# Kernel optimization log

Hardware: AMD Instinct MI355X
Metric: run time of the kernel (lower is better)

The kernel has to match this reference:

```python
import jax, jax.numpy as jnp
import numpy as np
from math import sqrt

B, D, H, HD, PF, K = 256, 1024, 8, 128, 2, 4
P = PF * D        # 2048, up-projected dim
HID = H * HD      # 1024
EPS = 1e-5


def _lin_w(key, out_d, in_d):
    return jax.random.normal(key, (out_d, in_d), jnp.float32) / np.sqrt(in_d)


def setup_inputs() -> dict:
    key = jax.random.key(0)
    ks = jax.random.split(key, 16)
    inp = {
        "seq": jax.random.normal(ks[0], (B, D), jnp.float32),
        "c_tm1": jax.random.normal(ks[1], (B, H, HD, HD), jnp.float32) * 0.1,
        "n_tm1": jnp.ones((B, H, HD), jnp.float32),
        "m_tm1": jnp.zeros((B, H), jnp.float32),
        # norms
        "ln_w": jnp.ones((D,), jnp.float32), "ln_b": jnp.zeros((D,), jnp.float32),
        "gn_w": jnp.ones((HID,), jnp.float32), "gn_b": jnp.zeros((HID,), jnp.float32),
        # linears (torch Linear: y = x @ W.T + b)
        "up_l_w": _lin_w(ks[2], P, D), "up_l_b": jnp.zeros((P,), jnp.float32),
        "up_r_w": _lin_w(ks[3], HID, D), "up_r_b": jnp.zeros((HID,), jnp.float32),
        "down_w": _lin_w(ks[4], D, HID), "down_b": jnp.zeros((D,), jnp.float32),
        "Wi_w": _lin_w(ks[5], H, P), "Wi_b": jnp.zeros((H,), jnp.float32),
        "Wf_w": _lin_w(ks[6], H, P), "Wf_b": jnp.zeros((H,), jnp.float32),
        "Wo_w": _lin_w(ks[7], HID, P), "Wo_b": jnp.zeros((HID,), jnp.float32),
        "Wq_w": _lin_w(ks[8], HID, P), "Wq_b": jnp.zeros((HID,), jnp.float32),
        "Wk_w": _lin_w(ks[9], HID, P), "Wk_b": jnp.zeros((HID,), jnp.float32),
        "Wv_w": _lin_w(ks[10], HID, P), "Wv_b": jnp.zeros((HID,), jnp.float32),
        # causal conv1d (1->1 channel, kernel K) and 1x1 skip conv (no bias)
        "conv_w": jax.random.normal(ks[11], (K,), jnp.float32) / np.sqrt(K),
        "conv_b": jnp.zeros((), jnp.float32),
        "skip_w": _lin_w(ks[12], HID, P),
    }
    return inp


def _layernorm(x, w, b):
    mu = jnp.mean(x, -1, keepdims=True)
    var = jnp.mean(jnp.square(x - mu), -1, keepdims=True)
    return (x - mu) * jax.lax.rsqrt(var + EPS) * w + b


def reference(seq, c_tm1, n_tm1, m_tm1, ln_w, ln_b, gn_w, gn_b,
              up_l_w, up_l_b, up_r_w, up_r_b, down_w, down_b,
              Wi_w, Wi_b, Wf_w, Wf_b, Wo_w, Wo_b,
              Wq_w, Wq_b, Wk_w, Wk_b, Wv_w, Wv_b,
              conv_w, conv_b, skip_w):
    x_n = _layernorm(seq, ln_w, ln_b)                     # [B, D]
    x_t = x_n @ up_l_w.T + up_l_b                         # [B, P]
    r_t = x_n @ up_r_w.T + up_r_b                         # [B, HID]

    # causal conv along feature axis: left-pad K-1, cross-correlate
    xp = jnp.pad(x_t, ((0, 0), (K - 1, 0)))
    x_c = sum(conv_w[j] * xp[:, j:j + P] for j in range(K)) + conv_b
    x_c = jax.nn.silu(x_c)                                # [B, P]

    q = (x_c @ Wq_w.T + Wq_b).reshape(B, H, HD)
    k = (x_c @ Wk_w.T + Wk_b).reshape(B, H, HD) / sqrt(HD)
    v = (x_t @ Wv_w.T + Wv_b).reshape(B, H, HD)
    i_t = x_c @ Wi_w.T + Wi_b                             # [B, H]
    f_t = x_c @ Wf_w.T + Wf_b                             # [B, H]
    o_t = jax.nn.sigmoid(x_t @ Wo_w.T + Wo_b)             # [B, HID]

    # stabilized exponential gating
    m_t = jnp.maximum(f_t + m_tm1, i_t)
    i_g = jnp.exp(i_t - m_t)
    f_g = jnp.exp(f_t - m_t + m_tm1)

    vk = jnp.einsum('bhd,bhp->bhdp', v, k)                # outer-product write
    c_t = f_g[:, :, None, None] * c_tm1 + i_g[:, :, None, None] * vk
    n_t = f_g[:, :, None] * n_tm1 + i_g[:, :, None] * k

    num = jnp.einsum('bhdp,bhp->bhd', c_t, q)
    den = jnp.maximum(jnp.einsum('bhd,bhd->bh', n_t, q), 1.0)
    h_t = o_t * (num / den[:, :, None]).reshape(B, HID)   # [B, HID]

    # GroupNorm(H groups) over channels
    hg = h_t.reshape(B, H, HD)
    mu = jnp.mean(hg, -1, keepdims=True)
    var = jnp.mean(jnp.square(hg - mu), -1, keepdims=True)
    hn = ((hg - mu) * jax.lax.rsqrt(var + EPS)).reshape(B, HID) * gn_w + gn_b

    out = hn + x_c @ skip_w.T                             # 1x1 skip conv
    out = out * jax.nn.silu(r_t)
    out = out @ down_w.T + down_b
    return out + seq, c_t, n_t, m_t
```

## Files before the change

### kernel.cpp

```cpp
#include <hip/hip_runtime.h>
#include <hip/hip_bf16.h>
#include <math.h>

#define B 256
#define D 1024
#define H 8
#define HD 128
#define P 2048
#define HID 1024
#define EPS 1e-5f

typedef __hip_bfloat16 bf16;
typedef short short8 __attribute__((ext_vector_type(8)));
typedef float f32x4 __attribute__((ext_vector_type(4)));

#define AS1C(p) ((const __attribute__((address_space(1))) void*)(p))
#define AS3(p)  ((__attribute__((address_space(3))) void*)(p))

__global__ __launch_bounds__(256) void zero_kernel(float* __restrict__ p) {
    const int i = blockIdx.x * 256 + threadIdx.x;
    ((float4*)p)[i] = float4{0.f, 0.f, 0.f, 0.f};
}

struct CvtSegs { const float* src[8]; bf16* dst[8]; };

__global__ __launch_bounds__(256) void convert_kernel(CvtSegs cs) {
    const int idx = blockIdx.x * 256 + threadIdx.x;
    const float* src; bf16* dst; int base;
    if      (idx <  524288) { src = cs.src[0]; dst = cs.dst[0]; base = 0; }
    else if (idx <  786432) { src = cs.src[1]; dst = cs.dst[1]; base = 524288; }
    else if (idx < 1310720) { src = cs.src[2]; dst = cs.dst[2]; base = 786432; }
    else if (idx < 1835008) { src = cs.src[3]; dst = cs.dst[3]; base = 1310720; }
    else if (idx < 2359296) { src = cs.src[4]; dst = cs.dst[4]; base = 1835008; }
    else if (idx < 2883584) { src = cs.src[5]; dst = cs.dst[5]; base = 2359296; }
    else if (idx < 3407872) { src = cs.src[6]; dst = cs.dst[6]; base = 2883584; }
    else                    { src = cs.src[7]; dst = cs.dst[7]; base = 3407872; }
    const int j = idx - base;
    const float4 v = ((const float4*)src)[j];
    union { bf16 h[4]; uint2 u; } tmp;
    tmp.h[0] = __float2bfloat16(v.x); tmp.h[1] = __float2bfloat16(v.y);
    tmp.h[2] = __float2bfloat16(v.z); tmp.h[3] = __float2bfloat16(v.w);
    *(uint2*)&dst[4 * j] = tmp.u;
}

__global__ __launch_bounds__(256) void ln_kernel(
    const float* __restrict__ seq, const float* __restrict__ w,
    const float* __restrict__ b, bf16* __restrict__ xn)
{
    const int row = blockIdx.x;
    const int tid = threadIdx.x;
    const int lane = tid & 63, wv = tid >> 6;
    const float* x = seq + (size_t)row * D;
    __shared__ float red[8];

    float vals[4];
    float s = 0.f, s2 = 0.f;
#pragma unroll
    for (int i = 0; i < 4; ++i) {
        float v = x[tid + 256 * i];
        vals[i] = v; s += v; s2 += v * v;
    }
#pragma unroll
    for (int off = 32; off; off >>= 1) {
        s  += __shfl_down(s, off, 64);
        s2 += __shfl_down(s2, off, 64);
    }
    if (lane == 0) { red[wv] = s; red[4 + wv] = s2; }
    __syncthreads();
    const float tot  = red[0] + red[1] + red[2] + red[3];
    const float tot2 = red[4] + red[5] + red[6] + red[7];
    const float mu = tot * (1.f / D);
    const float var = tot2 * (1.f / D) - mu * mu;
    const float rs = rsqrtf(var + EPS);
#pragma unroll
    for (int i = 0; i < 4; ++i) {
        const int c = tid + 256 * i;
        xn[(size_t)row * D + c] = __float2bfloat16((vals[i] - mu) * rs * w[c] + b[c]);
    }
}

struct Segs {
    const bf16* A[5];
    const bf16* W[5];
    float* O[5];
    int ostride[5];
};

__global__ __launch_bounds__(256) void gemm_bf16_sk(Segs segs, int K, int KS) {
    const int nt = blockIdx.x;
    const int seg = nt >> 4, nloc = nt & 15;
    const int m0 = blockIdx.y * 64;
    const int k0 = blockIdx.z * KS;
    const bf16* Ab = segs.A[seg];
    const bf16* Wb = segs.W[seg] + (size_t)(nloc * 64) * K;

    __shared__ bf16 As[2][64 * 64];
    __shared__ bf16 Bs[2][64 * 64];

    const int tid = threadIdx.x;
    const int srow = tid >> 3;
    const int scol = ((tid & 7) ^ (srow & 7)) * 8;
    const bf16* gA = Ab + (size_t)(m0 + srow) * K + k0 + scol;
    const bf16* gB = Wb + (size_t)srow * K + k0 + scol;
    const size_t rowK32 = (size_t)32 * K;

    const int lane = tid & 63, wave = tid >> 6;
    const int wm = (wave >> 1) * 32, wn = (wave & 1) * 32;
    const int fr = lane & 15, kq = lane >> 4;
    const int s0 = ((kq ^ (fr & 7)) * 8);
    const int aoff = (wm + fr) * 64 + s0;
    const int boff = (wn + fr) * 64 + s0;

    f32x4 acc00 = {0.f, 0.f, 0.f, 0.f};
    f32x4 acc01 = {0.f, 0.f, 0.f, 0.f};
    f32x4 acc10 = {0.f, 0.f, 0.f, 0.f};
    f32x4 acc11 = {0.f, 0.f, 0.f, 0.f};

    const int nIter = KS >> 6;

    __builtin_amdgcn_global_load_lds(AS1C(gA),          AS3(&As[0][tid * 8]),        16, 0, 0);
    __builtin_amdgcn_global_load_lds(AS1C(gA + rowK32), AS3(&As[0][2048 + tid * 8]), 16, 0, 0);
    __builtin_amdgcn_global_load_lds(AS1C(gB),          AS3(&Bs[0][tid * 8]),        16, 0, 0);
    __builtin_amdgcn_global_load_lds(AS1C(gB + rowK32), AS3(&Bs[0][2048 + tid * 8]), 16, 0, 0);

    int buf = 0;
    for (int it = 0; it < nIter; ++it) {
        __syncthreads();
        if (it + 1 < nIter) {
            const int ko = (it + 1) * 64;
            __builtin_amdgcn_global_load_lds(AS1C(gA + ko),          AS3(&As[buf ^ 1][tid * 8]),        16, 0, 0);
            __builtin_amdgcn_global_load_lds(AS1C(gA + ko + rowK32), AS3(&As[buf ^ 1][2048 + tid * 8]), 16, 0, 0);
            __builtin_amdgcn_global_load_lds(AS1C(gB + ko),          AS3(&Bs[buf ^ 1][tid * 8]),        16, 0, 0);
            __builtin_amdgcn_global_load_lds(AS1C(gB + ko + rowK32), AS3(&Bs[buf ^ 1][2048 + tid * 8]), 16, 0, 0);
        }
        {
            const short8 a0 = *(const short8*)&As[buf][aoff];
            const short8 a1 = *(const short8*)&As[buf][aoff + 1024];
            const short8 b0 = *(const short8*)&Bs[buf][boff];
            const short8 b1 = *(const short8*)&Bs[buf][boff + 1024];
            acc00 = __builtin_amdgcn_mfma_f32_16x16x32_bf16(a0, b0, acc00, 0, 0, 0);
            acc01 = __builtin_amdgcn_mfma_f32_16x16x32_bf16(a0, b1, acc01, 0, 0, 0);
            acc10 = __builtin_amdgcn_mfma_f32_16x16x32_bf16(a1, b0, acc10, 0, 0, 0);
            acc11 = __builtin_amdgcn_mfma_f32_16x16x32_bf16(a1, b1, acc11, 0, 0, 0);
        }
        {
            const short8 a0 = *(const short8*)&As[buf][aoff ^ 32];
            const short8 a1 = *(const short8*)&As[buf][(aoff + 1024) ^ 32];
            const short8 b0 = *(const short8*)&Bs[buf][boff ^ 32];
            const short8 b1 = *(const short8*)&Bs[buf][(boff + 1024) ^ 32];
            acc00 = __builtin_amdgcn_mfma_f32_16x16x32_bf16(a0, b0, acc00, 0, 0, 0);
            acc01 = __builtin_amdgcn_mfma_f32_16x16x32_bf16(a0, b1, acc01, 0, 0, 0);
            acc10 = __builtin_amdgcn_mfma_f32_16x16x32_bf16(a1, b0, acc10, 0, 0, 0);
            acc11 = __builtin_amdgcn_mfma_f32_16x16x32_bf16(a1, b1, acc11, 0, 0, 0);
        }
        buf ^= 1;
    }

    float* Ob = segs.O[seg] + nloc * 64 + wn;
    const int ost = segs.ostride[seg];
    const int r0 = m0 + wm + (lane >> 4) * 4;
    const int c0 = lane & 15;
#pragma unroll
    for (int r = 0; r < 4; ++r) {
        atomicAdd(&Ob[(size_t)(r0 + r) * ost + c0],           acc00[r]);
        atomicAdd(&Ob[(size_t)(r0 + r) * ost + 16 + c0],      acc01[r]);
        atomicAdd(&Ob[(size_t)(r0 + r + 16) * ost + c0],      acc10[r]);
        atomicAdd(&Ob[(size_t)(r0 + r + 16) * ost + 16 + c0], acc11[r]);
    }
}

__global__ __launch_bounds__(256) void conv_kernel(
    const float* __restrict__ xtacc, const float* __restrict__ ulb,
    const float* __restrict__ cw, const float* __restrict__ cb,
    bf16* __restrict__ xt_bf, float* __restrict__ xc, bf16* __restrict__ xc_bf)
{
    const int idx = blockIdx.x * 256 + threadIdx.x;
    const int b = idx >> 11, i = idx & 2047;
    const float* row = xtacc + (size_t)b * P;
    const float x0 = row[i] + ulb[i];
    xt_bf[idx] = __float2bfloat16(x0);
    float acc = cb[0] + cw[3] * x0;
    if (i >= 1) acc = fmaf(cw[2], row[i - 1] + ulb[i - 1], acc);
    if (i >= 2) acc = fmaf(cw[1], row[i - 2] + ulb[i - 2], acc);
    if (i >= 3) acc = fmaf(cw[0], row[i - 3] + ulb[i - 3], acc);
    const float sv = acc / (1.f + expf(-acc));
    xc[idx] = sv;
    xc_bf[idx] = __float2bfloat16(sv);
}

__global__ __launch_bounds__(256) void if_kernel(
    const float* __restrict__ xc,
    const float* __restrict__ Wi, const float* __restrict__ Wib,
    const float* __restrict__ Wf, const float* __restrict__ Wfb,
    float* __restrict__ it, float* __restrict__ ft)
{
    const int blk = blockIdx.x;
    const int b = blk >> 3, h = blk & 7;
    const int tid = threadIdx.x;
    const int lane = tid & 63, wv = tid >> 6;
    const float* x = xc + (size_t)b * P;
    const float* wi = Wi + (size_t)h * P;
    const float* wf = Wf + (size_t)h * P;
    float pi = 0.f, pf = 0.f;
    for (int p = tid; p < P; p += 256) {
        const float xv = x[p];
        pi = fmaf(xv, wi[p], pi);
        pf = fmaf(xv, wf[p], pf);
    }
    __shared__ float red[8];
#pragma unroll
    for (int off = 32; off; off >>= 1) {
        pi += __shfl_down(pi, off, 64);
        pf += __shfl_down(pf, off, 64);
    }
    if (lane == 0) { red[wv] = pi; red[4 + wv] = pf; }
    __syncthreads();
    if (tid == 0) {
        it[blk] = red[0] + red[1] + red[2] + red[3] + Wib[h];
        ft[blk] = red[4] + red[5] + red[6] + red[7] + Wfb[h];
    }
}

__global__ __launch_bounds__(256) void gate_kernel(
    const float* __restrict__ c_tm1, const float* __restrict__ n_tm1,
    const float* __restrict__ m_tm1, const float* __restrict__ it_a,
    const float* __restrict__ ft_a,
    const float* __restrict__ qacc, const float* __restrict__ kacc,
    const float* __restrict__ vacc, const float* __restrict__ oacc,
    const float* __restrict__ sacc, const float* __restrict__ racc,
    const float* __restrict__ qb, const float* __restrict__ kb,
    const float* __restrict__ vb, const float* __restrict__ ob,
    const float* __restrict__ rb,
    const float* __restrict__ gn_w, const float* __restrict__ gn_b,
    float* __restrict__ c_out, float* __restrict__ n_out,
    float* __restrict__ m_out, bf16* __restrict__ y)
{
    const int blk = blockIdx.x;
    const int b = blk >> 3, h = blk & 7;
    const int tid = threadIdx.x;
    const int lane = tid & 63, wv = tid >> 6;
    const float kscale = 0.08838834764831845f;

    __shared__ float sk_[128], sq_[128], sv_[128], snum[128];
    __shared__ float red[8];

    const float it = it_a[blk], ft = ft_a[blk], mp = m_tm1[blk];
    const float mt = fmaxf(ft + mp, it);
    const float ig = expf(it - mt);
    const float fg = expf(ft - mt + mp);
    if (tid == 0) m_out[blk] = mt;

    const int col0 = h * HD;
    const int hid_off = b * HID + col0;
    float den_p = 0.f;
    if (tid < 128) {
        const int col = col0 + tid;
        const float kd = (kacc[hid_off + tid] + kb[col]) * kscale;
        const float qd = qacc[hid_off + tid] + qb[col];
        sk_[tid] = kd; sq_[tid] = qd;
        sv_[tid] = vacc[hid_off + tid] + vb[col];
        const float nn = fg * n_tm1[(size_t)blk * HD + tid] + ig * kd;
        n_out[(size_t)blk * HD + tid] = nn;
        den_p = nn * qd;
    }
    __syncthreads();
#pragma unroll
    for (int off = 32; off; off >>= 1) den_p += __shfl_down(den_p, off, 64);
    if (lane == 0) red[wv] = den_p;
    __syncthreads();
    const float den = fmaxf(red[0] + red[1] + red[2] + red[3], 1.0f);

    const float k0 = sk_[2 * lane], k1 = sk_[2 * lane + 1];
    const float q0 = sq_[2 * lane], q1 = sq_[2 * lane + 1];
    const size_t cbase = (size_t)blk * (HD * HD);
#pragma unroll 4
    for (int r = 0; r < 32; ++r) {
        const int d = r * 4 + wv;
        const float2 c2 = *(const float2*)(c_tm1 + cbase + d * HD + 2 * lane);
        const float a = ig * sv_[d];
        const float c0v = fmaf(fg, c2.x, a * k0);
        const float c1v = fmaf(fg, c2.y, a * k1);
        float2 st; st.x = c0v; st.y = c1v;
        *(float2*)(c_out + cbase + d * HD + 2 * lane) = st;
        float psum = c0v * q0 + c1v * q1;
#pragma unroll
        for (int off = 32; off; off >>= 1) psum += __shfl_down(psum, off, 64);
        if (lane == 0) snum[d] = psum;
    }
    __syncthreads();

    float hval = 0.f, s1 = 0.f, s2 = 0.f;
    if (tid < 128) {
        const int col = col0 + tid;
        const float ot = 1.f / (1.f + expf(-(oacc[hid_off + tid] + ob[col])));
        hval = ot * snum[tid] / den;
        s1 = hval; s2 = hval * hval;
    }
#pragma unroll
    for (int off = 32; off; off >>= 1) {
        s1 += __shfl_down(s1, off, 64);
        s2 += __shfl_down(s2, off, 64);
    }
    if (lane == 0) { red[wv] = s1; red[4 + wv] = s2; }
    __syncthreads();
    const float mu = (red[0] + red[1] + red[2] + red[3]) * (1.f / HD);
    const float ms = (red[4] + red[5] + red[6] + red[7]) * (1.f / HD);
    const float var = ms - mu * mu;
    if (tid < 128) {
        const int col = col0 + tid;
        const float hn = (hval - mu) * rsqrtf(var + EPS) * gn_w[col] + gn_b[col];
        const float sr = racc[hid_off + tid] + rb[col];
        const float silu_r = sr / (1.f + expf(-sr));
        y[hid_off + tid] = __float2bfloat16((hn + sacc[hid_off + tid]) * silu_r);
    }
}

__global__ __launch_bounds__(256) void e3_kernel(
    const float* __restrict__ dacc, const float* __restrict__ db,
    const float* __restrict__ seq, float* __restrict__ out)
{
    const int i = blockIdx.x * 256 + threadIdx.x;
    const float4 d = ((const float4*)dacc)[i];
    const float4 s = ((const float4*)seq)[i];
    const float4 bb = ((const float4*)db)[i & 255];
    float4 o;
    o.x = d.x + s.x + bb.x; o.y = d.y + s.y + bb.y;
    o.z = d.z + s.z + bb.z; o.w = d.w + s.w + bb.w;
    ((float4*)out)[i] = o;
}

extern "C" void kernel_launch(void* const* d_in, const int* in_sizes, int n_in,
                              void* d_out, int out_size, void* d_ws, size_t ws_size,
                              hipStream_t stream) {
    const float* seq    = (const float*)d_in[0];
    const float* c_tm1  = (const float*)d_in[1];
    const float* n_tm1  = (const float*)d_in[2];
    const float* m_tm1  = (const float*)d_in[3];
    const float* ln_w   = (const float*)d_in[4];
    const float* ln_b   = (const float*)d_in[5];
    const float* gn_w   = (const float*)d_in[6];
    const float* gn_b   = (const float*)d_in[7];
    const float* up_l_w = (const float*)d_in[8];
    const float* up_l_b = (const float*)d_in[9];
    const float* up_r_w = (const float*)d_in[10];
    const float* up_r_b = (const float*)d_in[11];
    const float* down_w = (const float*)d_in[12];
    const float* down_b = (const float*)d_in[13];
    const float* Wi_w   = (const float*)d_in[14];
    const float* Wi_b   = (const float*)d_in[15];
    const float* Wf_w   = (const float*)d_in[16];
    const float* Wf_b   = (const float*)d_in[17];
    const float* Wo_w   = (const float*)d_in[18];
    const float* Wo_b   = (const float*)d_in[19];
    const float* Wq_w   = (const float*)d_in[20];
    const float* Wq_b   = (const float*)d_in[21];
    const float* Wk_w   = (const float*)d_in[22];
    const float* Wk_b   = (const float*)d_in[23];
    const float* Wv_w   = (const float*)d_in[24];
    const float* Wv_b   = (const float*)d_in[25];
    const float* conv_w = (const float*)d_in[26];
    const float* conv_b = (const float*)d_in[27];
    const float* skip_w = (const float*)d_in[28];

    float* ws = (float*)d_ws;
    float* xtacc = ws;
    float* racc  = ws + 524288;
    float* qacc  = ws + 786432;
    float* kacc  = ws + 1048576;
    float* vacc  = ws + 1310720;
    float* oacc  = ws + 1572864;
    float* sacc  = ws + 1835008;
    float* dacc  = ws + 2097152;
    float* itb   = ws + 2359296;
    float* ftb   = ws + 2361344;
    bf16* yb_bf   = (bf16*)(ws + 2363392);
    bf16* down_bf = (bf16*)(ws + 2494464);

    float* out0  = (float*)d_out;
    float* c_out = out0 + 262144;
    float* n_out = out0 + 33816576;
    float* m_out = out0 + 34078720;

    bf16* wbuf   = (bf16*)c_out;
    bf16* upl_bf = wbuf;
    bf16* upr_bf = wbuf + 2097152;
    bf16* wq_bf  = wbuf + 3145728;
    bf16* wk_bf  = wbuf + 5242880;
    bf16* wv_bf  = wbuf + 7340032;
    bf16* wo_bf  = wbuf + 9437184;
    bf16* wsk_bf = wbuf + 11534336;
    bf16* xn_bf  = wbuf + 13631488;
    bf16* xt_bf  = wbuf + 13893632;
    bf16* xc_bf  = wbuf + 14417920;
    float* xc_f  = (float*)(wbuf + 14942208);

    zero_kernel<<<2304, 256, 0, stream>>>(ws);

    CvtSegs cv;
    cv.src[0] = up_l_w; cv.dst[0] = upl_bf;
    cv.src[1] = up_r_w; cv.dst[1] = upr_bf;
    cv.src[2] = Wq_w;   cv.dst[2] = wq_bf;
    cv.src[3] = Wk_w;   cv.dst[3] = wk_bf;
    cv.src[4] = Wv_w;   cv.dst[4] = wv_bf;
    cv.src[5] = Wo_w;   cv.dst[5] = wo_bf;
    cv.src[6] = skip_w; cv.dst[6] = wsk_bf;
    cv.src[7] = down_w; cv.dst[7] = down_bf;
    convert_kernel<<<14336, 256, 0, stream>>>(cv);

    ln_kernel<<<B, 256, 0, stream>>>(seq, ln_w, ln_b, xn_bf);

    Segs g1{};
    g1.A[0] = xn_bf; g1.W[0] = upl_bf;               g1.O[0] = xtacc;        g1.ostride[0] = P;
    g1.A[1] = xn_bf; g1.W[1] = upl_bf + 1024 * 1024; g1.O[1] = xtacc + 1024; g1.ostride[1] = P;
    g1.A[2] = xn_bf; g1.W[2] = upr_bf;               g1.O[2] = racc;         g1.ostride[2] = HID;
    gemm_bf16_sk<<<dim3(48, 4, 4), 256, 0, stream>>>(g1, 1024, 256);

    conv_kernel<<<(B * P) / 256, 256, 0, stream>>>(
        xtacc, up_l_b, conv_w, conv_b, xt_bf, xc_f, xc_bf);

    Segs g2{};
    g2.A[0] = xc_bf; g2.W[0] = wq_bf;  g2.O[0] = qacc; g2.ostride[0] = HID;
    g2.A[1] = xc_bf; g2.W[1] = wk_bf;  g2.O[1] = kacc; g2.ostride[1] = HID;
    g2.A[2] = xt_bf; g2.W[2] = wv_bf;  g2.O[2] = vacc; g2.ostride[2] = HID;
    g2.A[3] = xt_bf; g2.W[3] = wo_bf;  g2.O[3] = oacc; g2.ostride[3] = HID;
    g2.A[4] = xc_bf; g2.W[4] = wsk_bf; g2.O[4] = sacc; g2.ostride[4] = HID;
    gemm_bf16_sk<<<dim3(80, 4, 2), 256, 0, stream>>>(g2, 2048, 1024);

    if_kernel<<<B * H, 256, 0, stream>>>(xc_f, Wi_w, Wi_b, Wf_w, Wf_b, itb, ftb);

    gate_kernel<<<B * H, 256, 0, stream>>>(
        c_tm1, n_tm1, m_tm1, itb, ftb,
        qacc, kacc, vacc, oacc, sacc, racc,
        Wq_b, Wk_b, Wv_b, Wo_b, up_r_b, gn_w, gn_b,
        c_out, n_out, m_out, yb_bf);

    Segs g3{};
    g3.A[0] = yb_bf; g3.W[0] = down_bf; g3.O[0] = dacc; g3.ostride[0] = HID;
    gemm_bf16_sk<<<dim3(16, 4, 4), 256, 0, stream>>>(g3, 1024, 256);

    e3_kernel<<<256, 256, 0, stream>>>(dacc, down_b, seq, out0);
}
```

Before: 393.4 us.

## Fuse fp32-to-bf16 weight conversion into GEMM loads and vectorize gate kernel

Drops the separate weight conversion kernel. The GEMM now loads fp32 weight tiles into registers, converts them to bf16 and writes them swizzled into LDS, overlapping this with the MFMA work through register prefetch. This avoids writing and re-reading about 14M bf16 weights each call. Split-K and M-tiling now re-read the fp32 weights (twice the bytes) several times. The gate kernel's c-state update also switches to float4 accesses with batched xor-shuffle row reductions.

```diff
diff --git a/kernel.cpp b/kernel.cpp
--- a/kernel.cpp
+++ b/kernel.cpp
@@ -20,27 +20,6 @@
 __global__ __launch_bounds__(256) void zero_kernel(float* __restrict__ p) {
     const int i = blockIdx.x * 256 + threadIdx.x;
     ((float4*)p)[i] = float4{0.f, 0.f, 0.f, 0.f};
-}
-
-struct CvtSegs { const float* src[8]; bf16* dst[8]; };
-
-__global__ __launch_bounds__(256) void convert_kernel(CvtSegs cs) {
-    const int idx = blockIdx.x * 256 + threadIdx.x;
-    const float* src; bf16* dst; int base;
-    if      (idx <  524288) { src = cs.src[0]; dst = cs.dst[0]; base = 0; }
-    else if (idx <  786432) { src = cs.src[1]; dst = cs.dst[1]; base = 524288; }
-    else if (idx < 1310720) { src = cs.src[2]; dst = cs.dst[2]; base = 786432; }
-    else if (idx < 1835008) { src = cs.src[3]; dst = cs.dst[3]; base = 1310720; }
-    else if (idx < 2359296) { src = cs.src[4]; dst = cs.dst[4]; base = 1835008; }
-    else if (idx < 2883584) { src = cs.src[5]; dst = cs.dst[5]; base = 2359296; }
-    else if (idx < 3407872) { src = cs.src[6]; dst = cs.dst[6]; base = 2883584; }
-    else                    { src = cs.src[7]; dst = cs.dst[7]; base = 3407872; }
-    const int j = idx - base;
-    const float4 v = ((const float4*)src)[j];
-    union { bf16 h[4]; uint2 u; } tmp;
-    tmp.h[0] = __float2bfloat16(v.x); tmp.h[1] = __float2bfloat16(v.y);
-    tmp.h[2] = __float2bfloat16(v.z); tmp.h[3] = __float2bfloat16(v.w);
-    *(uint2*)&dst[4 * j] = tmp.u;
 }
 
 __global__ __launch_bounds__(256) void ln_kernel(
@@ -81,10 +60,19 @@
 
 struct Segs {
     const bf16* A[5];
-    const bf16* W[5];
+    const float* W[5];
     float* O[5];
     int ostride[5];
 };
+
+static __device__ inline short8 cvt8(float4 a, float4 b) {
+    union { bf16 h[8]; short8 s; } u;
+    u.h[0] = __float2bfloat16(a.x); u.h[1] = __float2bfloat16(a.y);
+    u.h[2] = __float2bfloat16(a.z); u.h[3] = __float2bfloat16(a.w);
+    u.h[4] = __float2bfloat16(b.x); u.h[5] = __float2bfloat16(b.y);
+    u.h[6] = __float2bfloat16(b.z); u.h[7] = __float2bfloat16(b.w);
+    return u.s;
+}
 
 __global__ __launch_bounds__(256) void gemm_bf16_sk(Segs segs, int K, int KS) {
     const int nt = blockIdx.x;
@@ -92,17 +80,20 @@
     const int m0 = blockIdx.y * 64;
     const int k0 = blockIdx.z * KS;
     const bf16* Ab = segs.A[seg];
-    const bf16* Wb = segs.W[seg] + (size_t)(nloc * 64) * K;
+    const float* Wb = segs.W[seg] + (size_t)(nloc * 64) * K;
 
     __shared__ bf16 As[2][64 * 64];
     __shared__ bf16 Bs[2][64 * 64];
 
     const int tid = threadIdx.x;
     const int srow = tid >> 3;
-    const int scol = ((tid & 7) ^ (srow & 7)) * 8;
-    const bf16* gA = Ab + (size_t)(m0 + srow) * K + k0 + scol;
-    const bf16* gB = Wb + (size_t)srow * K + k0 + scol;
+    const int swz8 = ((tid & 7) ^ (srow & 7)) * 8;
+    const bf16* gA = Ab + (size_t)(m0 + srow) * K + k0 + swz8;
     const size_t rowK32 = (size_t)32 * K;
+    const float* gW0 = Wb + (size_t)srow * K + k0 + (tid & 7) * 8;
+    const float* gW1 = gW0 + rowK32;
+    const int wd0 = srow * 64 + swz8;
+    const int wd1 = (srow + 32) * 64 + swz8;
 
     const int lane = tid & 63, wave = tid >> 6;
     const int wm = (wave >> 1) * 32, wn = (wave & 1) * 32;
@@ -118,20 +109,26 @@
 
     const int nIter = KS >> 6;
 
+    float4 w00 = *(const float4*)(gW0);
+    float4 w01 = *(const float4*)(gW0 + 4);
+    float4 w10 = *(const float4*)(gW1);
+    float4 w11 = *(const float4*)(gW1 + 4);
     __builtin_amdgcn_global_load_lds(AS1C(gA),          AS3(&As[0][tid * 8]),        16, 0, 0);
     __builtin_amdgcn_global_load_lds(AS1C(gA + rowK32), AS3(&As[0][2048 + tid * 8]), 16, 0, 0);
-    __builtin_amdgcn_global_load_lds(AS1C(gB),          AS3(&Bs[0][tid * 8]),        16, 0, 0);
-    __builtin_amdgcn_global_load_lds(AS1C(gB + rowK32), AS3(&Bs[0][2048 + tid * 8]), 16, 0, 0);
+    *(short8*)&Bs[0][wd0] = cvt8(w00, w01);
+    *(short8*)&Bs[0][wd1] = cvt8(w10, w11);
 
     int buf = 0;
     for (int it = 0; it < nIter; ++it) {
         __syncthreads();
         if (it + 1 < nIter) {
             const int ko = (it + 1) * 64;
+            w00 = *(const float4*)(gW0 + ko);
+            w01 = *(const float4*)(gW0 + ko + 4);
+            w10 = *(const float4*)(gW1 + ko);
+            w11 = *(const float4*)(gW1 + ko + 4);
             __builtin_amdgcn_global_load_lds(AS1C(gA + ko),          AS3(&As[buf ^ 1][tid * 8]),        16, 0, 0);
             __builtin_amdgcn_global_load_lds(AS1C(gA + ko + rowK32), AS3(&As[buf ^ 1][2048 + tid * 8]), 16, 0, 0);
-            __builtin_amdgcn_global_load_lds(AS1C(gB + ko),          AS3(&Bs[buf ^ 1][tid * 8]),        16, 0, 0);
-            __builtin_amdgcn_global_load_lds(AS1C(gB + ko + rowK32), AS3(&Bs[buf ^ 1][2048 + tid * 8]), 16, 0, 0);
         }
         {
             const short8 a0 = *(const short8*)&As[buf][aoff];
@@ -153,6 +150,10 @@
             acc10 = __builtin_amdgcn_mfma_f32_16x16x32_bf16(a1, b0, acc10, 0, 0, 0);
             acc11 = __builtin_amdgcn_mfma_f32_16x16x32_bf16(a1, b1, acc11, 0, 0, 0);
         }
+        if (it + 1 < nIter) {
+            *(short8*)&Bs[buf ^ 1][wd0] = cvt8(w00, w01);
+            *(short8*)&Bs[buf ^ 1][wd1] = cvt8(w10, w11);
+        }
         buf ^= 1;
     }
 
@@ -241,7 +242,10 @@
     const int lane = tid & 63, wv = tid >> 6;
     const float kscale = 0.08838834764831845f;
 
-    __shared__ float sk_[128], sq_[128], sv_[128], snum[128];
+    __shared__ __align__(16) float sk_[128];
+    __shared__ __align__(16) float sq_[128];
+    __shared__ __align__(16) float sv_[128];
+    __shared__ __align__(16) float snum[128];
     __shared__ float red[8];
 
     const float it = it_a[blk], ft = ft_a[blk], mp = m_tm1[blk];
@@ -270,22 +274,36 @@
     __syncthreads();
     const float den = fmaxf(red[0] + red[1] + red[2] + red[3], 1.0f);
 
-    const float k0 = sk_[2 * lane], k1 = sk_[2 * lane + 1];
-    const float q0 = sq_[2 * lane], q1 = sq_[2 * lane + 1];
+    const int cchunk = tid & 31;
+    const int a0r = tid >> 5;
+    const float4 k4 = *(const float4*)&sk_[cchunk * 4];
+    const float4 q4 = *(const float4*)&sq_[cchunk * 4];
     const size_t cbase = (size_t)blk * (HD * HD);
-#pragma unroll 4
-    for (int r = 0; r < 32; ++r) {
-        const int d = r * 4 + wv;
-        const float2 c2 = *(const float2*)(c_tm1 + cbase + d * HD + 2 * lane);
-        const float a = ig * sv_[d];
-        const float c0v = fmaf(fg, c2.x, a * k0);
-        const float c1v = fmaf(fg, c2.y, a * k1);
-        float2 st; st.x = c0v; st.y = c1v;
-        *(float2*)(c_out + cbase + d * HD + 2 * lane) = st;
-        float psum = c0v * q0 + c1v * q1;
-#pragma unroll
-        for (int off = 32; off; off >>= 1) psum += __shfl_down(psum, off, 64);
-        if (lane == 0) snum[d] = psum;
+    const float4* cin4 = (const float4*)(c_tm1 + cbase);
+    float4* cout4 = (float4*)(c_out + cbase);
+    float part[16];
+#pragma unroll
+    for (int j = 0; j < 16; ++j) {
+        const int m = tid + 256 * j;
+        const int row = a0r + 8 * j;
+        const float av = ig * sv_[row];
+        float4 c4 = cin4[m];
+        c4.x = fmaf(fg, c4.x, av * k4.x);
+        c4.y = fmaf(fg, c4.y, av * k4.y);
+        c4.z = fmaf(fg, c4.z, av * k4.z);
+        c4.w = fmaf(fg, c4.w, av * k4.w);
+        cout4[m] = c4;
+        part[j] = c4.x * q4.x + c4.y * q4.y + c4.z * q4.z + c4.w * q4.w;
+    }
+#pragma unroll
+    for (int j = 0; j < 16; ++j) {
+        float p = part[j];
+        p += __shfl_xor(p, 1, 64);
+        p += __shfl_xor(p, 2, 64);
+        p += __shfl_xor(p, 4, 64);
+        p += __shfl_xor(p, 8, 64);
+        p += __shfl_xor(p, 16, 64);
+        if (cchunk == j) snum[a0r + 8 * j] = p;
     }
     __syncthreads();
 
@@ -373,8 +391,7 @@
     float* dacc  = ws + 2097152;
     float* itb   = ws + 2359296;
     float* ftb   = ws + 2361344;
-    bf16* yb_bf   = (bf16*)(ws + 2363392);
-    bf16* down_bf = (bf16*)(ws + 2494464);
+    bf16* yb_bf  = (bf16*)(ws + 2363392);
 
     float* out0  = (float*)d_out;
     float* c_out = out0 + 262144;
@@ -382,48 +399,30 @@
     float* m_out = out0 + 34078720;
 
     bf16* wbuf   = (bf16*)c_out;
-    bf16* upl_bf = wbuf;
-    bf16* upr_bf = wbuf + 2097152;
-    bf16* wq_bf  = wbuf + 3145728;
-    bf16* wk_bf  = wbuf + 5242880;
-    bf16* wv_bf  = wbuf + 7340032;
-    bf16* wo_bf  = wbuf + 9437184;
-    bf16* wsk_bf = wbuf + 11534336;
-    bf16* xn_bf  = wbuf + 13631488;
-    bf16* xt_bf  = wbuf + 13893632;
-    bf16* xc_bf  = wbuf + 14417920;
-    float* xc_f  = (float*)(wbuf + 14942208);
+    bf16* xn_bf  = wbuf;
+    bf16* xt_bf  = wbuf + 262144;
+    bf16* xc_bf  = wbuf + 786432;
+    float* xc_f  = (float*)(wbuf + 1310720);
 
     zero_kernel<<<2304, 256, 0, stream>>>(ws);
 
-    CvtSegs cv;
-    cv.src[0] = up_l_w; cv.dst[0] = upl_bf;
-    cv.src[1] = up_r_w; cv.dst[1] = upr_bf;
-    cv.src[2] = Wq_w;   cv.dst[2] = wq_bf;
-    cv.src[3] = Wk_w;   cv.dst[3] = wk_bf;
-    cv.src[4] = Wv_w;   cv.dst[4] = wv_bf;
-    cv.src[5] = Wo_w;   cv.dst[5] = wo_bf;
-    cv.src[6] = skip_w; cv.dst[6] = wsk_bf;
-    cv.src[7] = down_w; cv.dst[7] = down_bf;
-    convert_kernel<<<14336, 256, 0, stream>>>(cv);
-
     ln_kernel<<<B, 256, 0, stream>>>(seq, ln_w, ln_b, xn_bf);
 
     Segs g1{};
-    g1.A[0] = xn_bf; g1.W[0] = upl_bf;               g1.O[0] = xtacc;        g1.ostride[0] = P;
-    g1.A[1] = xn_bf; g1.W[1] = upl_bf + 1024 * 1024; g1.O[1] = xtacc + 1024; g1.ostride[1] = P;
-    g1.A[2] = xn_bf; g1.W[2] = upr_bf;               g1.O[2] = racc;         g1.ostride[2] = HID;
+    g1.A[0] = xn_bf; g1.W[0] = up_l_w;               g1.O[0] = xtacc;        g1.ostride[0] = P;
+    g1.A[1] = xn_bf; g1.W[1] = up_l_w + 1024 * 1024; g1.O[1] = xtacc + 1024; g1.ostride[1] = P;
+    g1.A[2] = xn_bf; g1.W[2] = up_r_w;               g1.O[2] = racc;         g1.ostride[2] = HID;
     gemm_bf16_sk<<<dim3(48, 4, 4), 256, 0, stream>>>(g1, 1024, 256);
 
     conv_kernel<<<(B * P) / 256, 256, 0, stream>>>(
         xtacc, up_l_b, conv_w, conv_b, xt_bf, xc_f, xc_bf);
 
     Segs g2{};
-    g2.A[0] = xc_bf; g2.W[0] = wq_bf;  g2.O[0] = qacc; g2.ostride[0] = HID;
-    g2.A[1] = xc_bf; g2.W[1] = wk_bf;  g2.O[1] = kacc; g2.ostride[1] = HID;
-    g2.A[2] = xt_bf; g2.W[2] = wv_bf;  g2.O[2] = vacc; g2.ostride[2] = HID;
-    g2.A[3] = xt_bf; g2.W[3] = wo_bf;  g2.O[3] = oacc; g2.ostride[3] = HID;
-    g2.A[4] = xc_bf; g2.W[4] = wsk_bf; g2.O[4] = sacc; g2.ostride[4] = HID;
+    g2.A[0] = xc_bf; g2.W[0] = Wq_w;   g2.O[0] = qacc; g2.ostride[0] = HID;
+    g2.A[1] = xc_bf; g2.W[1] = Wk_w;   g2.O[1] = kacc; g2.ostride[1] = HID;
+    g2.A[2] = xt_bf; g2.W[2] = Wv_w;   g2.O[2] = vacc; g2.ostride[2] = HID;
+    g2.A[3] = xt_bf; g2.W[3] = Wo_w;   g2.O[3] = oacc; g2.ostride[3] = HID;
+    g2.A[4] = xc_bf; g2.W[4] = skip_w; g2.O[4] = sacc; g2.ostride[4] = HID;
     gemm_bf16_sk<<<dim3(80, 4, 2), 256, 0, stream>>>(g2, 2048, 1024);
 
     if_kernel<<<B * H, 256, 0, stream>>>(xc_f, Wi_w, Wi_b, Wf_w, Wf_b, itb, ftb);
@@ -435,7 +434,7 @@
         c_out, n_out, m_out, yb_bf);
 
     Segs g3{};
-    g3.A[0] = yb_bf; g3.W[0] = down_bf; g3.O[0] = dacc; g3.ostride[0] = HID;
+    g3.A[0] = yb_bf; g3.W[0] = down_w; g3.O[0] = dacc; g3.ostride[0] = HID;
     gemm_bf16_sk<<<dim3(16, 4, 4), 256, 0, stream>>>(g3, 1024, 256);
 
     e3_kernel<<<256, 256, 0, stream>>>(dacc, down_b, seq, out0);
```

After: 393.4 us. About the same (+0.0%).
